# Kernel optimization log

Measured on AMD Instinct MI355X. Metric: run time of the kernel, lower is better.

The kernel has to match this reference:

```python
import jax, jax.numpy as jnp
import numpy as np

LEAK = 0.2
TEMP = 0.1          # CausalMask temperature
SPARSITY_W = 0.1
MI_W = 0.01
DAG_W = 1.0

def _leaky(x):
    return jax.nn.leaky_relu(x, LEAK)

def setup_inputs() -> dict:
    key = jax.random.key(0)
    B, F, S, H = 4096, 512, 32, 512
    H2, CH = H // 2, 64
    P = S * (S - 1) // 2  # 496 MI estimators
    ks = jax.random.split(key, 32)
    def w(k, shape, fan_in):
        return jax.random.normal(k, shape, jnp.float32) / np.sqrt(fan_in)
    return {
        'features': jax.random.normal(ks[0], (B, F), jnp.float32),
        'eps':      jax.random.normal(ks[1], (B, S), jnp.float32),
        'enc_w1': w(ks[2], (F, H), F),   'enc_b1': w(ks[3], (H,), H),
        'enc_w2': w(ks[4], (H, 2 * S), H), 'enc_b2': w(ks[5], (2 * S,), H) * 0.1,
        'log_weight': jax.random.normal(ks[6], (S, S), jnp.float32) * 0.5,
        'mech_w1': w(ks[7], (S, S, H2), S), 'mech_b1': w(ks[8], (S, H2), H2),
        'mech_w2': w(ks[9], (S, H2), H2),   'mech_b2': w(ks[10], (S,), H2),
        'dec_w1': w(ks[11], (S, H), S),  'dec_b1': w(ks[12], (H,), H),
        'dec_w2': w(ks[13], (H, F), H),  'dec_b2': w(ks[14], (F,), H),
        'mi_w1': w(ks[15], (P, 2, CH), 2),  'mi_b1': w(ks[16], (P, CH), CH),
        'mi_w2': w(ks[17], (P, CH, CH), CH), 'mi_b2': w(ks[18], (P, CH), CH),
        'mi_w3': w(ks[19], (P, CH), CH),     'mi_b3': w(ks[20], (P,), CH),
    }

def _forward(features, eps, enc_w1, enc_b1, enc_w2, enc_b2, log_weight,
             mech_w1, mech_b1, mech_w2, mech_b2, dec_w1, dec_b1, dec_w2, dec_b2,
             mi_w1, mi_b1, mi_w2, mi_b2, mi_w3, mi_b3):
    S = log_weight.shape[0]
    # ---- encode ----
    h = _leaky(features @ enc_w1 + enc_b1)
    params = h @ enc_w2 + enc_b2
    mean, log_std = jnp.split(params, 2, axis=-1)
    std = jnp.exp(log_std)
    z = mean + std * eps                                   # [B,S]
    # ---- soft causal adjacency (training mode) ----
    eye = jnp.eye(S, dtype=features.dtype)
    upper = jnp.triu(jnp.ones((S, S), features.dtype), k=1)
    lw = log_weight * upper - 10.0 * eye
    A = jax.nn.sigmoid(lw / TEMP)                          # [S,S]
    # ---- apply_causal_structure: stoch_dim tiny MLPs, vectorized ----
    # z_parents[b,i,s] = z[b,s] * A[s,i]
    zp = z[:, None, :] * A.T[None, :, :]                   # [B,S,S]
    h1 = _leaky(jnp.einsum('bis,ish->bih', zp, mech_w1) + mech_b1)  # [B,S,H2]
    z_causal = jnp.einsum('bih,ih->bi', h1, mech_w2) + mech_b2      # [B,S]
    # ---- decode ----
    recon = _leaky(z_causal @ dec_w1 + dec_b1) @ dec_w2 + dec_b2    # [B,F]
    # ---- losses ----
    recon_loss = jnp.mean((recon - features) ** 2)
    kl_loss = 0.5 * jnp.sum(mean ** 2 + std ** 2 - 2.0 * log_std - 1.0, axis=-1).mean()
    Asig = jax.nn.sigmoid(log_weight)
    sparsity_loss = jnp.sum(jnp.abs(Asig))
    # MI: one tiny MLP per (i<j) pair, row-major order == torch loop order
    iu, ju = jnp.triu_indices(S, k=1)
    pair = jnp.stack([z[:, iu], z[:, ju]], axis=-1)        # [B,P,2]
    m1 = _leaky(jnp.einsum('bpi,pih->bph', pair, mi_w1) + mi_b1)
    m2 = _leaky(jnp.einsum('bph,phk->bpk', m1, mi_w2) + mi_b2)
    mi_est = (jnp.einsum('bph,ph->bp', m2, mi_w3) + mi_b3).mean(0)  # [P]
    mi_loss = jnp.sum(jax.nn.sigmoid(log_weight[iu, ju]) * mi_est)
    # DAG: truncated matrix-exponential trace penalty
    A2 = Asig * Asig
    expm = eye
    mp = eye
    fact = 1.0
    for i in range(1, 10):
        fact *= i
        mp = mp @ A2
        expm = expm + mp / fact
    dag_loss = (jnp.trace(expm) - S) ** 2
    total_loss = recon_loss + kl_loss + SPARSITY_W * sparsity_loss + MI_W * mi_loss + DAG_W * dag_loss
    return z_causal, mean, std, recon, total_loss, recon_loss, kl_loss, sparsity_loss, mi_loss, dag_loss

def reference(features, eps, enc_w1, enc_b1, enc_w2, enc_b2, log_weight,
              mech_w1, mech_b1, mech_w2, mech_b2, dec_w1, dec_b1, dec_w2, dec_b2,
              mi_w1, mi_b1, mi_w2, mi_b2, mi_w3, mi_b3):
    return _forward(features, eps, enc_w1, enc_b1, enc_w2, enc_b2, log_weight,
                    mech_w1, mech_b1, mech_w2, mech_b2, dec_w1, dec_b1, dec_w2, dec_b2,
                    mi_w1, mi_b1, mi_w2, mi_b2, mi_w3, mi_b3)
```

## Files before the change

kernel.cpp:

```cpp
#include <hip/hip_runtime.h>
#include <hip/hip_bf16.h>

typedef float f32x4 __attribute__((ext_vector_type(4)));
typedef float f32x2 __attribute__((ext_vector_type(2)));
typedef short s16x8 __attribute__((ext_vector_type(8)));

__device__ __forceinline__ float leaky2(float x){ return fmaf(0.4f, fabsf(x), 0.6f * x); }

__device__ __forceinline__ short f2bf(float f){
    return __builtin_bit_cast(short, __float2bfloat16(f));
}

__global__ __launch_bounds__(256) void k_cvt(
    const float* __restrict__ feat, const float* __restrict__ ew1,
    const float* __restrict__ ew2, const float* __restrict__ dw2,
    const float* __restrict__ mw1, const float* __restrict__ mw2,
    const float* __restrict__ dw1,
    short* __restrict__ featbf, short* __restrict__ w1p,
    short* __restrict__ ew2p, short* __restrict__ dw2p,
    short* __restrict__ mw1p, short* __restrict__ mw2p,
    short* __restrict__ dw1p,
    const float* __restrict__ lw, float* __restrict__ A,
    float* __restrict__ acc)
{
    if (blockIdx.x >= 2048){
        __shared__ float A2s[1024], mp[1024], red[256];
        const int t = threadIdx.x;
        float part = 0.f;
        #pragma unroll
        for (int q = 0; q < 4; ++q){
            int e = t * 4 + q;
            int r = e >> 5, c = e & 31;
            float v = lw[e];
            float sig = 1.f / (1.f + expf(-v));
            float l2 = (r < c) ? v * 10.f : ((r == c) ? -100.f : 0.f);
            A[e] = 1.f / (1.f + expf(-l2));
            part += sig;
            float a2 = sig * sig;
            A2s[e] = a2; mp[e] = a2;
        }
        red[t] = part; __syncthreads();
        for (int s = 128; s > 0; s >>= 1){ if (t < s) red[t] += red[t + s]; __syncthreads(); }
        if (t == 0) acc[2] = red[0];

        const float invf[10] = {0.f, 1.f, 0.5f, 1.6666667e-1f, 4.1666667e-2f,
                                8.3333333e-3f, 1.3888889e-3f, 1.9841270e-4f,
                                2.4801587e-5f, 2.7557319e-6f};
        float tr = 0.f;
        const int r = t >> 3, c0 = (t & 7) * 4;
        for (int n = 1; n <= 9; ++n){
            __syncthreads();
            if (t == 0){
                float s = 0.f;
                for (int k2 = 0; k2 < 32; ++k2) s += mp[k2 * 33];
                tr += s * invf[n];
            }
            if (n == 9) break;
            float av[4] = {0.f, 0.f, 0.f, 0.f};
            for (int k2 = 0; k2 < 32; ++k2){
                float m = mp[r * 32 + k2];
                #pragma unroll
                for (int q = 0; q < 4; ++q) av[q] = fmaf(m, A2s[k2 * 32 + c0 + q], av[q]);
            }
            __syncthreads();
            #pragma unroll
            for (int q = 0; q < 4; ++q) mp[r * 32 + c0 + q] = av[q];
        }
        if (t == 0) acc[3] = tr * tr;
        return;
    }
    for (int idx = blockIdx.x * 256 + threadIdx.x; idx < 4964352; idx += 2048 * 256){
        if (idx < 2097152){ featbf[idx] = f2bf(feat[idx]); continue; }
        int s = idx - 2097152;
        if (s < 262144){
            int k = s >> 9, n = s & 511;
            int lane = (((k >> 3) & 3) << 4) | (n & 15);
            w1p[((n >> 4) * 16 + (k >> 5)) * 512 + lane * 8 + (k & 7)] = f2bf(ew1[s]);
            continue;
        }
        s -= 262144;
        if (s < 32768){
            int k = s >> 6, n = s & 63;
            int lane = (((k >> 3) & 3) << 4) | (n & 15);
            ew2p[((n >> 4) * 16 + (k >> 5)) * 512 + lane * 8 + (k & 7)] = f2bf(ew2[s]);
            continue;
        }
        s -= 32768;
        if (s < 262144){
            int k = s >> 9, n = s & 511;
            int lane = (((k >> 3) & 3) << 4) | (n & 15);
            dw2p[((n >> 4) * 16 + (k >> 5)) * 512 + lane * 8 + (k & 7)] = f2bf(dw2[s]);
            continue;
        }
        s -= 262144;
        if (s < 262144){
            int i = s >> 13, r2 = s & 8191;
            int k = r2 >> 8, n = r2 & 255;
            int lane = (((k >> 3) & 3) << 4) | (n & 15);
            mw1p[i * 8192 + (n >> 4) * 512 + lane * 8 + (k & 7)] = f2bf(mw1[s]);
            continue;
        }
        s -= 262144;
        if (s < 2031616){
            int p = s >> 12, r2 = s & 4095;
            int k = r2 >> 6, n = r2 & 63;
            int lane = (((k >> 3) & 3) << 4) | (n & 15);
            mw2p[p * 4096 + ((n >> 4) * 2 + (k >> 5)) * 512 + lane * 8 + (k & 7)] = f2bf(mw2[s]);
            continue;
        }
        s -= 2031616;
        int k = s >> 9, n = s & 511;
        int lane = (((k >> 3) & 3) << 4) | (n & 15);
        dw1p[(n >> 4) * 512 + lane * 8 + (k & 7)] = f2bf(dw1[s]);
    }
}

__global__ __launch_bounds__(256) void k_encf(
    const short* __restrict__ featbf, const short* __restrict__ w1p,
    const float* __restrict__ eb1, const short* __restrict__ ew2p,
    const float* __restrict__ eb2, const float* __restrict__ eps,
    float* __restrict__ omean, float* __restrict__ ostd,
    float* __restrict__ zt, float* __restrict__ accg)
{
    __shared__ short hlds[8192];
    __shared__ float P[16][65];
    __shared__ float zs[16][33];
    __shared__ float red[256];
    const int t = threadIdx.x, lane = t & 63, wv = t >> 6;
    const int ml = lane & 15, kg = lane >> 4;
    const int b0 = blockIdx.x * 16;

    f32x4 acc1[8] = {};
    for (int kt = 0; kt < 16; ++kt){
        s16x8 a = *(const s16x8*)&featbf[(size_t)(b0 + ml) * 512 + kt * 32 + kg * 8];
        #pragma unroll
        for (int nf = 0; nf < 8; ++nf){
            s16x8 b = *(const s16x8*)&w1p[((wv * 8 + nf) * 16 + kt) * 512 + lane * 8];
            acc1[nf] = __builtin_amdgcn_mfma_f32_16x16x32_bf16(a, b, acc1[nf], 0, 0, 0);
        }
    }
    #pragma unroll
    for (int nf = 0; nf < 8; ++nf){
        int col = wv * 128 + nf * 16 + ml;
        float bv = eb1[col];
        #pragma unroll
        for (int r = 0; r < 4; ++r){
            int row = kg * 4 + r;
            int byte = (row * 1024 + col * 2) ^ ((row & 7) << 4);
            hlds[byte >> 1] = f2bf(leaky2(acc1[nf][r] + bv));
        }
    }
    __syncthreads();

    f32x4 acc2 = {};
    for (int kt = 0; kt < 16; ++kt){
        int byte = (ml * 1024 + kt * 64 + kg * 16) ^ ((ml & 7) << 4);
        s16x8 a = *(const s16x8*)((const char*)hlds + byte);
        s16x8 b = *(const s16x8*)&ew2p[(wv * 16 + kt) * 512 + lane * 8];
        acc2 = __builtin_amdgcn_mfma_f32_16x16x32_bf16(a, b, acc2, 0, 0, 0);
    }
    {
        int col = wv * 16 + ml;
        float bv = eb2[col];
        #pragma unroll
        for (int r = 0; r < 4; ++r)
            P[kg * 4 + r][col] = acc2[r] + bv;
    }
    __syncthreads();
    float klp = 0.f;
    #pragma unroll
    for (int q = 0; q < 2; ++q){
        int e = q * 256 + t;
        int row = e >> 5, n = e & 31;
        float mean = P[row][n], ls = P[row][n + 32];
        float sd = expf(ls);
        size_t o = (size_t)(b0 + row) * 32 + n;
        float z = fmaf(sd, eps[o], mean);
        omean[o] = mean; ostd[o] = sd;
        zs[row][n] = z;
        klp += mean * mean + sd * sd - 2.f * ls - 1.f;
    }
    __syncthreads();
    #pragma unroll
    for (int q = 0; q < 2; ++q){
        int e = q * 256 + t;
        int n = e >> 4, row = e & 15;
        zt[(size_t)n * 4096 + b0 + row] = zs[row][n];
    }
    red[t] = klp; __syncthreads();
    for (int s = 128; s > 0; s >>= 1){ if (t < s) red[t] += red[t + s]; __syncthreads(); }
    if (t == 0) atomicAdd(accg + 0, red[0]);
}

__global__ __launch_bounds__(256) void k_mimech(
    const float* __restrict__ zt,
    const float* __restrict__ w1g, const float* __restrict__ b1g,
    const short* __restrict__ w2p, const float* __restrict__ b2g,
    const float* __restrict__ w3g, float* __restrict__ macc,
    const float* __restrict__ A, const short* __restrict__ W1p,
    const float* __restrict__ mb1, const float* __restrict__ mw2,
    const float* __restrict__ mb2, float* __restrict__ out_zc)
{
    __shared__ float sA[32], sB1[256], sW2[256];
    const int t = threadIdx.x, lane = t & 63, wv = t >> 6;
    const int ml = lane & 15, kg = lane >> 4;
    if (blockIdx.x < 1984){
        const int p = blockIdx.x >> 2, bq = blockIdx.x & 3;
        int pi = 0, rem = p;
        while (rem >= 31 - pi){ rem -= 31 - pi; ++pi; }
        const int pj = pi + 1 + rem;

        const int zrow = wv * 16 + ml;
        const float* zi_b = zt + (size_t)pi * 4096 + bq * 1024 + zrow;
        const float* zj_b = zt + (size_t)pj * 4096 + bq * 1024 + zrow;

        f32x2 w10v[2][4], w11v[2][4], b1v[2][4];
        #pragma unroll
        for (int ks = 0; ks < 2; ++ks)
            #pragma unroll
            for (int q = 0; q < 4; ++q){
                int h = ks * 32 + kg * 8 + q * 2;
                w10v[ks][q] = *(const f32x2*)&w1g[p * 128 + h] * 0.6f;
                w11v[ks][q] = *(const f32x2*)&w1g[p * 128 + 64 + h] * 0.6f;
                b1v[ks][q]  = *(const f32x2*)&b1g[p * 64 + h] * 0.6f;
            }
        s16x8 bfr[4][2];
        f32x4 b2c[4];
        #pragma unroll
        for (int nb = 0; nb < 4; ++nb){
            float bv = b2g[p * 64 + nb * 16 + ml];
            b2c[nb][0] = bv; b2c[nb][1] = bv; b2c[nb][2] = bv; b2c[nb][3] = bv;
            #pragma unroll
            for (int ks = 0; ks < 2; ++ks)
                bfr[nb][ks] = *(const s16x8*)&w2p[(size_t)p * 4096 + (nb * 2 + ks) * 512 + lane * 8];
        }
        const f32x2 c23 = {0.66666669f, 0.66666669f};
        float slin[4] = {0.f, 0.f, 0.f, 0.f}, sabs[4] = {0.f, 0.f, 0.f, 0.f};
        #pragma unroll 1
        for (int tile = 0; tile < 16; ++tile){
            float zi_c = zi_b[tile * 64], zj_c = zj_b[tile * 64];
            f32x2 zi2 = {zi_c, zi_c}, zj2 = {zj_c, zj_c};
            s16x8 af0, af1;
            #pragma unroll
            for (int q = 0; q < 4; ++q){
                f32x2 m0 = __builtin_elementwise_fma(zi2, w10v[0][q],
                           __builtin_elementwise_fma(zj2, w11v[0][q], b1v[0][q]));
                m0 = __builtin_elementwise_fma(c23, __builtin_elementwise_abs(m0), m0);
                af0[q * 2] = f2bf(m0[0]); af0[q * 2 + 1] = f2bf(m0[1]);
                f32x2 m1 = __builtin_elementwise_fma(zi2, w10v[1][q],
                           __builtin_elementwise_fma(zj2, w11v[1][q], b1v[1][q]));
                m1 = __builtin_elementwise_fma(c23, __builtin_elementwise_abs(m1), m1);
                af1[q * 2] = f2bf(m1[0]); af1[q * 2 + 1] = f2bf(m1[1]);
            }
            #pragma unroll
            for (int nb = 0; nb < 4; ++nb){
                f32x4 d = __builtin_amdgcn_mfma_f32_16x16x32_bf16(af0, bfr[nb][0], b2c[nb], 0, 0, 0);
                d = __builtin_amdgcn_mfma_f32_16x16x32_bf16(af1, bfr[nb][1], d, 0, 0, 0);
                #pragma unroll
                for (int r2 = 0; r2 < 4; ++r2){
                    slin[nb] += d[r2];
                    sabs[nb] += fabsf(d[r2]);
                }
            }
        }
        float s = 0.f;
        #pragma unroll
        for (int nb = 0; nb < 4; ++nb){
            float w3 = w3g[p * 64 + nb * 16 + ml];
            s = fmaf(0.6f * w3, slin[nb], fmaf(0.4f * w3, sabs[nb], s));
        }
        #pragma unroll
        for (int off = 32; off; off >>= 1) s += __shfl_xor(s, off);
        if (lane == 0) atomicAdd(&macc[p], s);
    } else {
        const int bx = blockIdx.x - 1984;
        const int i = bx & 31;
        const int b0 = (bx >> 5) * 64 + wv * 16;
        if (t < 32) sA[t] = A[t * 32 + i];
        sB1[t] = mb1[i * 256 + t];
        sW2[t] = mw2[i * 256 + t];
        __syncthreads();
        float zv[8];
        #pragma unroll
        for (int q = 0; q < 8; ++q)
            zv[q] = zt[(size_t)(kg * 8 + q) * 4096 + b0 + ml];
        s16x8 af;
        #pragma unroll
        for (int q = 0; q < 8; ++q)
            af[q] = f2bf(zv[q] * sA[kg * 8 + q]);
        float s[4] = {0.f, 0.f, 0.f, 0.f};
        #pragma unroll
        for (int nt = 0; nt < 16; ++nt){
            s16x8 bf = *(const s16x8*)&W1p[i * 8192 + nt * 512 + lane * 8];
            int col = nt * 16 + ml;
            float b1e = sB1[col], w2v = sW2[col];
            f32x4 d;
            d[0] = b1e; d[1] = b1e; d[2] = b1e; d[3] = b1e;
            d = __builtin_amdgcn_mfma_f32_16x16x32_bf16(af, bf, d, 0, 0, 0);
            float w2a = 0.6f * w2v, w2b = 0.4f * w2v;
            #pragma unroll
            for (int r = 0; r < 4; ++r)
                s[r] = fmaf(w2a, d[r], fmaf(w2b, fabsf(d[r]), s[r]));
        }
        #pragma unroll
        for (int off = 1; off < 16; off <<= 1)
            #pragma unroll
            for (int r = 0; r < 4; ++r) s[r] += __shfl_xor(s[r], off);
        if (ml == 0){
            float bb = mb2[i];
            #pragma unroll
            for (int r = 0; r < 4; ++r){
                int b = b0 + kg * 4 + r;
                out_zc[(size_t)b * 32 + i] = s[r] + bb;
            }
        }
    }
}

__global__ __launch_bounds__(256) void k_decf(
    const float* __restrict__ zc, const short* __restrict__ dw1p,
    const float* __restrict__ db1, const short* __restrict__ dw2p,
    const float* __restrict__ db2, const float* __restrict__ feat,
    float* __restrict__ recon, float* __restrict__ accg)
{
    __shared__ short dlds[16384];
    __shared__ float red[256];
    const int t = threadIdx.x, lane = t & 63, wv = t >> 6;
    const int ml = lane & 15, kg = lane >> 4;
    const int b0 = blockIdx.x * 32;
    const int c0 = blockIdx.y * 128;

    s16x8 af[2];
    #pragma unroll
    for (int m = 0; m < 2; ++m){
        int row = b0 + m * 16 + ml;
        f32x4 z0 = *(const f32x4*)&zc[(size_t)row * 32 + kg * 8];
        f32x4 z1 = *(const f32x4*)&zc[(size_t)row * 32 + kg * 8 + 4];
        #pragma unroll
        for (int e = 0; e < 4; ++e){
            af[m][e] = f2bf(z0[e]);
            af[m][e + 4] = f2bf(z1[e]);
        }
    }
    #pragma unroll
    for (int nf = 0; nf < 8; ++nf){
        int nt = wv * 8 + nf;
        s16x8 bf = *(const s16x8*)&dw1p[nt * 512 + lane * 8];
        int col = nt * 16 + ml;
        float b1e = db1[col];
        f32x4 c; c[0] = b1e; c[1] = b1e; c[2] = b1e; c[3] = b1e;
        #pragma unroll
        for (int m = 0; m < 2; ++m){
            f32x4 d = __builtin_amdgcn_mfma_f32_16x16x32_bf16(af[m], bf, c, 0, 0, 0);
            #pragma unroll
            for (int r = 0; r < 4; ++r){
                int row = m * 16 + kg * 4 + r;
                int byte = (row * 1024 + col * 2) ^ ((row & 7) << 4);
                dlds[byte >> 1] = f2bf(leaky2(d[r]));
            }
        }
    }
    __syncthreads();

    f32x4 acc[2][2] = {};
    for (int kt = 0; kt < 16; ++kt){
        s16x8 a[2];
        #pragma unroll
        for (int m = 0; m < 2; ++m){
            int row = m * 16 + ml;
            int byte = (row * 1024 + kt * 64 + kg * 16) ^ ((row & 7) << 4);
            a[m] = *(const s16x8*)((const char*)dlds + byte);
        }
        #pragma unroll
        for (int j = 0; j < 2; ++j){
            int nt = (c0 >> 4) + wv * 2 + j;
            s16x8 b = *(const s16x8*)&dw2p[(nt * 16 + kt) * 512 + lane * 8];
            #pragma unroll
            for (int m = 0; m < 2; ++m)
                acc[m][j] = __builtin_amdgcn_mfma_f32_16x16x32_bf16(a[m], b, acc[m][j], 0, 0, 0);
        }
    }
    float lsum = 0.f;
    #pragma unroll
    for (int j = 0; j < 2; ++j){
        int col = c0 + (wv * 2 + j) * 16 + ml;
        float bv = db2[col];
        #pragma unroll
        for (int m = 0; m < 2; ++m)
            #pragma unroll
            for (int r = 0; r < 4; ++r){
                int row = b0 + m * 16 + kg * 4 + r;
                float v = acc[m][j][r] + bv;
                float d = v - feat[(size_t)row * 512 + col];
                lsum = fmaf(d, d, lsum);
                recon[(size_t)row * 512 + col] = v;
            }
    }
    red[t] = lsum; __syncthreads();
    for (int s = 128; s > 0; s >>= 1){ if (t < s) red[t] += red[t + s]; __syncthreads(); }
    if (t == 0) atomicAdd(accg + 1, red[0]);
}

__global__ void k_final(const float* __restrict__ acc, const float* __restrict__ lw,
                        const float* __restrict__ b3, float* __restrict__ outs)
{
    __shared__ float red[512];
    int t = threadIdx.x;
    float c = 0.f;
    if (t < 496){
        int pi = 0, rem = t;
        while (rem >= 31 - pi){ rem -= 31 - pi; ++pi; }
        int pj = pi + 1 + rem;
        float est = acc[4 + t] * (1.f / 4096.f) + b3[t];
        float w = 1.f / (1.f + expf(-lw[pi * 32 + pj]));
        c = w * est;
    }
    red[t] = c; __syncthreads();
    for (int s = 256; s > 0; s >>= 1){ if (t < s) red[t] += red[t + s]; __syncthreads(); }
    if (t == 0){
        float mi    = red[0];
        float recon = acc[1] * (1.f / (4096.f * 512.f));
        float kl    = 0.5f * acc[0] * (1.f / 4096.f);
        float sp    = acc[2], dag = acc[3];
        outs[0] = recon + kl + 0.1f * sp + 0.01f * mi + dag;
        outs[1] = recon; outs[2] = kl; outs[3] = sp; outs[4] = mi; outs[5] = dag;
    }
}

extern "C" void kernel_launch(void* const* d_in, const int* in_sizes, int n_in,
                              void* d_out, int out_size, void* d_ws, size_t ws_size,
                              hipStream_t stream)
{
    const float* features = (const float*)d_in[0];
    const float* eps      = (const float*)d_in[1];
    const float* enc_w1   = (const float*)d_in[2];
    const float* enc_b1   = (const float*)d_in[3];
    const float* enc_w2   = (const float*)d_in[4];
    const float* enc_b2   = (const float*)d_in[5];
    const float* log_w    = (const float*)d_in[6];
    const float* mech_w1  = (const float*)d_in[7];
    const float* mech_b1  = (const float*)d_in[8];
    const float* mech_w2  = (const float*)d_in[9];
    const float* mech_b2  = (const float*)d_in[10];
    const float* dec_w1   = (const float*)d_in[11];
    const float* dec_b1   = (const float*)d_in[12];
    const float* dec_w2   = (const float*)d_in[13];
    const float* dec_b2   = (const float*)d_in[14];
    const float* mi_w1    = (const float*)d_in[15];
    const float* mi_b1    = (const float*)d_in[16];
    const float* mi_w2    = (const float*)d_in[17];
    const float* mi_b2    = (const float*)d_in[18];
    const float* mi_w3    = (const float*)d_in[19];
    const float* mi_b3    = (const float*)d_in[20];

    float* W      = (float*)d_ws;
    float* zt     = W;
    float* Abuf   = W + 262144;
    float* accums = W + 263168;
    short* w1p    = (short*)(W + 263680);
    short* ew2p   = (short*)(W + 394752);
    short* dw2p   = (short*)(W + 411136);
    short* mw1p   = (short*)(W + 542208);
    short* mw2p   = (short*)(W + 673280);
    short* dw1p   = (short*)(W + 1689088);
    float* out    = (float*)d_out;
    short* featbf = (short*)(out + 393216);

    hipMemsetAsync(accums, 0, 512 * sizeof(float), stream);
    k_cvt<<<2049, 256, 0, stream>>>(features, enc_w1, enc_w2, dec_w2, mech_w1, mi_w2,
                                    dec_w1, featbf, w1p, ew2p, dw2p, mw1p, mw2p, dw1p,
                                    log_w, Abuf, accums);
    k_encf<<<256, 256, 0, stream>>>(featbf, w1p, enc_b1, ew2p, enc_b2, eps,
                                    out + 131072, out + 262144, zt, accums);
    k_mimech<<<4032, 256, 0, stream>>>(zt, mi_w1, mi_b1, mw2p, mi_b2, mi_w3, accums + 4,
                                       Abuf, mw1p, mech_b1, mech_w2, mech_b2, out);
    k_decf<<<dim3(128, 4), 256, 0, stream>>>(out, dw1p, dec_b1, dw2p, dec_b2, features,
                                             out + 393216, accums);
    k_final<<<1, 512, 0, stream>>>(accums, log_w, mi_b3, out + 2490368);
}
```

Baseline: 129.5 us.

## Compute MI first layer with MFMA and accumulate linear sum via MFMA

The first MI-estimator layer (two inputs plus bias) moves from per-lane FMA arithmetic onto MFMA instructions. A pre-permuted bf16 weight fragment packs w1 and b1, and a B operand carries zi, zj and a constant 1. The linear part of the second-layer sum is now accumulated by extra MFMAs instead of per-element adds, with the bias added back at the end. This cuts VALU work in the hot loop but adds more MFMAs, rounds z to bf16 (a small precision loss), and grows the conversion kernel with a new permuted weight buffer.

```diff
diff --git a/kernel.cpp b/kernel.cpp
--- a/kernel.cpp
+++ b/kernel.cpp
@@ -2,8 +2,8 @@
 #include <hip/hip_bf16.h>
 
 typedef float f32x4 __attribute__((ext_vector_type(4)));
-typedef float f32x2 __attribute__((ext_vector_type(2)));
 typedef short s16x8 __attribute__((ext_vector_type(8)));
+typedef unsigned u32x4 __attribute__((ext_vector_type(4)));
 
 __device__ __forceinline__ float leaky2(float x){ return fmaf(0.4f, fabsf(x), 0.6f * x); }
 
@@ -15,11 +15,12 @@
     const float* __restrict__ feat, const float* __restrict__ ew1,
     const float* __restrict__ ew2, const float* __restrict__ dw2,
     const float* __restrict__ mw1, const float* __restrict__ mw2,
-    const float* __restrict__ dw1,
+    const float* __restrict__ dw1, const float* __restrict__ miw1,
+    const float* __restrict__ mib1,
     short* __restrict__ featbf, short* __restrict__ w1p,
     short* __restrict__ ew2p, short* __restrict__ dw2p,
     short* __restrict__ mw1p, short* __restrict__ mw2p,
-    short* __restrict__ dw1p,
+    short* __restrict__ dw1p, short* __restrict__ wperm,
     const float* __restrict__ lw, float* __restrict__ A,
     float* __restrict__ acc)
 {
@@ -69,7 +70,7 @@
         if (t == 0) acc[3] = tr * tr;
         return;
     }
-    for (int idx = blockIdx.x * 256 + threadIdx.x; idx < 4964352; idx += 2048 * 256){
+    for (int idx = blockIdx.x * 256 + threadIdx.x; idx < 5980160; idx += 2048 * 256){
         if (idx < 2097152){ featbf[idx] = f2bf(feat[idx]); continue; }
         int s = idx - 2097152;
         if (s < 262144){
@@ -109,9 +110,24 @@
             continue;
         }
         s -= 2031616;
-        int k = s >> 9, n = s & 511;
-        int lane = (((k >> 3) & 3) << 4) | (n & 15);
-        dw1p[(n >> 4) * 512 + lane * 8 + (k & 7)] = f2bf(dw1[s]);
+        if (s < 16384){
+            int k = s >> 9, n = s & 511;
+            int lane = (((k >> 3) & 3) << 4) | (n & 15);
+            dw1p[(n >> 4) * 512 + lane * 8 + (k & 7)] = f2bf(dw1[s]);
+            continue;
+        }
+        s -= 16384;
+        int p = s >> 11, r2 = s & 2047;
+        int g = r2 >> 9, ln = (r2 >> 3) & 63, e = r2 & 7;
+        int kg = ln >> 4, ml2 = ln & 15;
+        float val = 0.f;
+        if (kg == 0 && e < 3){
+            int h = 32 * (g >> 1) + 8 * (ml2 >> 2) + 4 * (g & 1) + (ml2 & 3);
+            val = 0.6f * (e == 0 ? miw1[p * 128 + h]
+                        : e == 1 ? miw1[p * 128 + 64 + h]
+                                 : mib1[p * 64 + h]);
+        }
+        wperm[s] = f2bf(val);
     }
 }
 
@@ -194,7 +210,7 @@
 
 __global__ __launch_bounds__(256) void k_mimech(
     const float* __restrict__ zt,
-    const float* __restrict__ w1g, const float* __restrict__ b1g,
+    const short* __restrict__ wperm,
     const short* __restrict__ w2p, const float* __restrict__ b2g,
     const float* __restrict__ w3g, float* __restrict__ macc,
     const float* __restrict__ A, const short* __restrict__ W1p,
@@ -214,16 +230,10 @@
         const float* zi_b = zt + (size_t)pi * 4096 + bq * 1024 + zrow;
         const float* zj_b = zt + (size_t)pj * 4096 + bq * 1024 + zrow;
 
-        f32x2 w10v[2][4], w11v[2][4], b1v[2][4];
-        #pragma unroll
-        for (int ks = 0; ks < 2; ++ks)
-            #pragma unroll
-            for (int q = 0; q < 4; ++q){
-                int h = ks * 32 + kg * 8 + q * 2;
-                w10v[ks][q] = *(const f32x2*)&w1g[p * 128 + h] * 0.6f;
-                w11v[ks][q] = *(const f32x2*)&w1g[p * 128 + 64 + h] * 0.6f;
-                b1v[ks][q]  = *(const f32x2*)&b1g[p * 64 + h] * 0.6f;
-            }
+        s16x8 wfr[4];
+        #pragma unroll
+        for (int g = 0; g < 4; ++g)
+            wfr[g] = *(const s16x8*)&wperm[((size_t)p * 4 + g) * 512 + lane * 8];
         s16x8 bfr[4][2];
         f32x4 b2c[4];
         #pragma unroll
@@ -234,40 +244,50 @@
             for (int ks = 0; ks < 2; ++ks)
                 bfr[nb][ks] = *(const s16x8*)&w2p[(size_t)p * 4096 + (nb * 2 + ks) * 512 + lane * 8];
         }
-        const f32x2 c23 = {0.66666669f, 0.66666669f};
-        float slin[4] = {0.f, 0.f, 0.f, 0.f}, sabs[4] = {0.f, 0.f, 0.f, 0.f};
+        f32x4 accL[4] = {};
+        float sabs[4] = {0.f, 0.f, 0.f, 0.f};
         #pragma unroll 1
         for (int tile = 0; tile < 16; ++tile){
             float zi_c = zi_b[tile * 64], zj_c = zj_b[tile * 64];
-            f32x2 zi2 = {zi_c, zi_c}, zj2 = {zj_c, zj_c};
+            u32x4 bz32 = {0u, 0u, 0u, 0u};
+            unsigned lo = (unsigned)(unsigned short)f2bf(zi_c)
+                        | ((unsigned)(unsigned short)f2bf(zj_c) << 16);
+            bz32[0] = (kg == 0) ? lo : 0u;
+            bz32[1] = (kg == 0) ? 0x00003F80u : 0u;
+            s16x8 bz = __builtin_bit_cast(s16x8, bz32);
+            f32x4 zero = {0.f, 0.f, 0.f, 0.f};
+            f32x4 d1[4];
+            #pragma unroll
+            for (int g = 0; g < 4; ++g)
+                d1[g] = __builtin_amdgcn_mfma_f32_16x16x32_bf16(wfr[g], bz, zero, 0, 0, 0);
             s16x8 af0, af1;
             #pragma unroll
-            for (int q = 0; q < 4; ++q){
-                f32x2 m0 = __builtin_elementwise_fma(zi2, w10v[0][q],
-                           __builtin_elementwise_fma(zj2, w11v[0][q], b1v[0][q]));
-                m0 = __builtin_elementwise_fma(c23, __builtin_elementwise_abs(m0), m0);
-                af0[q * 2] = f2bf(m0[0]); af0[q * 2 + 1] = f2bf(m0[1]);
-                f32x2 m1 = __builtin_elementwise_fma(zi2, w10v[1][q],
-                           __builtin_elementwise_fma(zj2, w11v[1][q], b1v[1][q]));
-                m1 = __builtin_elementwise_fma(c23, __builtin_elementwise_abs(m1), m1);
-                af1[q * 2] = f2bf(m1[0]); af1[q * 2 + 1] = f2bf(m1[1]);
+            for (int g = 0; g < 4; ++g){
+                #pragma unroll
+                for (int r = 0; r < 4; ++r){
+                    float m = fmaf(0.66666669f, fabsf(d1[g][r]), d1[g][r]);
+                    short v = f2bf(m);
+                    if ((g >> 1) == 0) af0[(g & 1) * 4 + r] = v;
+                    else               af1[(g & 1) * 4 + r] = v;
+                }
             }
             #pragma unroll
             for (int nb = 0; nb < 4; ++nb){
                 f32x4 d = __builtin_amdgcn_mfma_f32_16x16x32_bf16(af0, bfr[nb][0], b2c[nb], 0, 0, 0);
                 d = __builtin_amdgcn_mfma_f32_16x16x32_bf16(af1, bfr[nb][1], d, 0, 0, 0);
-                #pragma unroll
-                for (int r2 = 0; r2 < 4; ++r2){
-                    slin[nb] += d[r2];
-                    sabs[nb] += fabsf(d[r2]);
-                }
+                accL[nb] = __builtin_amdgcn_mfma_f32_16x16x32_bf16(af0, bfr[nb][0], accL[nb], 0, 0, 0);
+                accL[nb] = __builtin_amdgcn_mfma_f32_16x16x32_bf16(af1, bfr[nb][1], accL[nb], 0, 0, 0);
+                sabs[nb] += fabsf(d[0]); sabs[nb] += fabsf(d[1]);
+                sabs[nb] += fabsf(d[2]); sabs[nb] += fabsf(d[3]);
             }
         }
         float s = 0.f;
         #pragma unroll
         for (int nb = 0; nb < 4; ++nb){
+            float slin = accL[nb][0] + accL[nb][1] + accL[nb][2] + accL[nb][3]
+                       + 64.f * b2c[nb][0];
             float w3 = w3g[p * 64 + nb * 16 + ml];
-            s = fmaf(0.6f * w3, slin[nb], fmaf(0.4f * w3, sabs[nb], s));
+            s = fmaf(0.6f * w3, slin, fmaf(0.4f * w3, sabs[nb], s));
         }
         #pragma unroll
         for (int off = 32; off; off >>= 1) s += __shfl_xor(s, off);
@@ -463,16 +483,18 @@
     short* mw1p   = (short*)(W + 542208);
     short* mw2p   = (short*)(W + 673280);
     short* dw1p   = (short*)(W + 1689088);
+    short* wperm  = (short*)(W + 1697280);
     float* out    = (float*)d_out;
     short* featbf = (short*)(out + 393216);
 
     hipMemsetAsync(accums, 0, 512 * sizeof(float), stream);
     k_cvt<<<2049, 256, 0, stream>>>(features, enc_w1, enc_w2, dec_w2, mech_w1, mi_w2,
-                                    dec_w1, featbf, w1p, ew2p, dw2p, mw1p, mw2p, dw1p,
+                                    dec_w1, mi_w1, mi_b1,
+                                    featbf, w1p, ew2p, dw2p, mw1p, mw2p, dw1p, wperm,
                                     log_w, Abuf, accums);
     k_encf<<<256, 256, 0, stream>>>(featbf, w1p, enc_b1, ew2p, enc_b2, eps,
                                     out + 131072, out + 262144, zt, accums);
-    k_mimech<<<4032, 256, 0, stream>>>(zt, mi_w1, mi_b1, mw2p, mi_b2, mi_w3, accums + 4,
+    k_mimech<<<4032, 256, 0, stream>>>(zt, wperm, mw2p, mi_b2, mi_w3, accums + 4,
                                        Abuf, mw1p, mech_b1, mech_w2, mech_b2, out);
     k_decf<<<dim3(128, 4), 256, 0, stream>>>(out, dw1p, dec_b1, dw2p, dec_b2, features,
                                              out + 393216, accums);
```

New measurement: 138.0 us. 1.07x slower.
